# Optimization experiments

Measured on AMD Instinct MI355X. Metric: run time of the kernel, lower is better.

Reference implementation:

```python
import jax, jax.numpy as jnp
import numpy as np

B, N, M, C, H = 8, 2048, 1024, 512, 8
D = C // H  # per-head dim = 64


def setup_inputs() -> dict:
    key = jax.random.key(0)
    ks = jax.random.split(key, 4)
    x = jax.random.normal(ks[0], (B, N, C), dtype=jnp.float32)
    global_tokens = jax.random.normal(ks[1], (B, M, C), dtype=jnp.float32)
    Wq = jax.random.normal(ks[2], (C, C), dtype=jnp.float32) * 0.02
    bq = jnp.zeros((C,), dtype=jnp.float32)
    Wkv = jax.random.normal(ks[3], (C, 2 * C), dtype=jnp.float32) * 0.02
    bkv = jnp.zeros((2 * C,), dtype=jnp.float32)
    return {"x": x, "global_tokens": global_tokens, "Wq": Wq, "bq": bq,
            "Wkv": Wkv, "bkv": bkv}


def reference(x, global_tokens, Wq, bq, Wkv, bkv):
    # q from x, k/v from global_tokens (LinearProjection with query=True)
    q = (x @ Wq + bq).reshape(B, N, H, D).transpose(0, 2, 1, 3)        # [B,H,N,D]
    kv = (global_tokens @ Wkv + bkv).reshape(B, M, 2, H, D)
    k = kv[:, :, 0].transpose(0, 2, 1, 3)                              # [B,H,M,D]
    v = kv[:, :, 1].transpose(0, 2, 1, 3)                              # [B,H,M,D]
    # NOTE: original module applies no 1/sqrt(D) scaling in forward
    attn = jnp.einsum('bhnd,bhmd->bhnm', q, k)                         # [B,H,N,M]
    attn = jax.nn.softmax(attn, axis=-1)
    out = jnp.einsum('bhnm,bhmd->bhnd', attn, v)                       # [B,H,N,D]
    return out.transpose(0, 2, 1, 3).reshape(B, N, C)
```

## Files before the change

kernel.cpp:

```cpp
#include <hip/hip_runtime.h>
#include <hip/hip_bf16.h>


typedef __bf16 bf16_t;
typedef __bf16 bf16x8 __attribute__((ext_vector_type(8)));
typedef __bf16 bf16x4 __attribute__((ext_vector_type(4)));
typedef float floatx16 __attribute__((ext_vector_type(16)));
typedef unsigned int uintx4 __attribute__((ext_vector_type(4)));
typedef unsigned int uintx2 __attribute__((ext_vector_type(2)));

#define KDIM 512
#define QSCALE 1.44269504088896f

__device__ __forceinline__ unsigned pack2(float a, float b) {
  unsigned short ua = __builtin_bit_cast(unsigned short, (bf16_t)a);
  unsigned short ub = __builtin_bit_cast(unsigned short, (bf16_t)b);
  return (unsigned)ua | ((unsigned)ub << 16);
}

__device__ __forceinline__ float fexp2(float x) {
#if __has_builtin(__builtin_amdgcn_exp2f)
  return __builtin_amdgcn_exp2f(x);
#else
  return __exp2f(x);
#endif
}

__device__ __forceinline__ bf16x8 cvt8(const float4 a, const float4 b) {
  bf16x8 r;
  r[0] = (bf16_t)a.x; r[1] = (bf16_t)a.y; r[2] = (bf16_t)a.z; r[3] = (bf16_t)a.w;
  r[4] = (bf16_t)b.x; r[5] = (bf16_t)b.y; r[6] = (bf16_t)b.z; r[7] = (bf16_t)b.w;
  return r;
}

__device__ __forceinline__ void gl_lds16(const bf16_t* g, bf16_t* l) {
#if __has_builtin(__builtin_amdgcn_global_load_lds)
  __builtin_amdgcn_global_load_lds(
      (const __attribute__((address_space(1))) unsigned int*)(g),
      (__attribute__((address_space(3))) unsigned int*)(l), 16, 0, 0);
#else
  *(bf16x8*)l = *(const bf16x8*)g;
#endif
}

__global__ __launch_bounds__(256) void prep_kernel(
    const float* __restrict__ Wq, const float* __restrict__ Wkv,
    const float* __restrict__ x, const float* __restrict__ gt,
    bf16_t* __restrict__ Wqt, bf16_t* __restrict__ Wkvt,
    bf16_t* __restrict__ Aq, bf16_t* __restrict__ Akv) {
  __shared__ float tile[64][65];
  const int blk = blockIdx.x;
  const int t = threadIdx.x;
  if (blk < 192) {
    const float* in; bf16_t* out; int N, bx, by;
    if (blk < 64) { in = Wq; out = Wqt; N = 512; bx = blk & 7; by = blk >> 3; }
    else { int t2 = blk - 64; in = Wkv; out = Wkvt; N = 1024; bx = t2 & 15; by = t2 >> 4; }
    const int c0 = bx * 64, k0 = by * 64;
#pragma unroll
    for (int i = 0; i < 16; ++i) {
      int idx = t + i * 256;
      int kk = idx >> 6, cc = idx & 63;
      tile[kk][cc] = in[(size_t)(k0 + kk) * N + (c0 + cc)];
    }
    __syncthreads();
#pragma unroll
    for (int j = 0; j < 2; ++j) {
      int unit = t + j * 256;
      int cc = unit >> 3, ks = (unit & 7) * 8;
      int c = c0 + cc, k = k0 + ks;
      bf16x8 v;
#pragma unroll
      for (int i = 0; i < 8; ++i) v[i] = (bf16_t)tile[ks + i][cc];
      const int k5 = k & 31;
      const int chunk = ((c & 127) >> 5) * 2 + (k5 >> 4);
      *(bf16x8*)(&out[(size_t)((c >> 7) * 16 + (k >> 5)) * 4096 + chunk * 512 +
                      (c & 31) * 8 + ((k5 >> 3) & 1) * 256]) = v;
    }
  } else {
    int idx = blk - 192;
    const float* src; bf16_t* dst; int rt, kt2;
    if (idx < 2048) { src = x; dst = Aq; rt = idx >> 4; kt2 = idx & 15; }
    else { int i2 = idx - 2048; src = gt; dst = Akv; rt = i2 >> 4; kt2 = i2 & 15; }
    const int row = rt * 128 + (t >> 1);
    const int kb = kt2 * 32 + (t & 1) * 16;
    const float* p = src + (size_t)row * KDIM + kb;
    float4 f0 = *(const float4*)(p);
    float4 f1 = *(const float4*)(p + 4);
    float4 f2 = *(const float4*)(p + 8);
    float4 f3 = *(const float4*)(p + 12);
    bf16x8 o0 = cvt8(f0, f1), o1 = cvt8(f2, f3);
    const int chunk = ((row & 127) >> 5) * 2 + (t & 1);
    bf16_t* ob = dst + (size_t)(rt * 16 + kt2) * 4096 + chunk * 512 + (row & 31) * 8;
    *(bf16x8*)(ob) = o0;
    *(bf16x8*)(ob + 256) = o1;
  }
}

__global__ __launch_bounds__(256) void proj_gemm_kernel(
    const bf16_t* __restrict__ Aq, const bf16_t* __restrict__ Akv,
    const bf16_t* __restrict__ Wqt, const bf16_t* __restrict__ Wkvt,
    const float* __restrict__ bq, const float* __restrict__ bkv,
    bf16_t* __restrict__ Qf, bf16_t* __restrict__ Kf, bf16_t* __restrict__ Vf) {
  __shared__ bf16_t lds[2][8192];
  const int blk = blockIdx.x;
  int mode, bx, by;
  const bf16_t* Ab; const bf16_t* Wb; const float* bias;
  if (blk < 512) { mode = 0; bx = blk & 3; by = blk >> 2; Ab = Aq; Wb = Wqt; bias = bq; }
  else { int tt = blk - 512; mode = 1; bx = tt & 7; by = tt >> 3; Ab = Akv; Wb = Wkvt; bias = bkv; }

  const int tid = threadIdx.x;
  const int wave = tid >> 6, L = tid & 63;
  const int l5 = L & 31, hf = L >> 5;
  const int wr = wave >> 1, wc = wave & 1;
  const int rb = by * 128, cb = bx * 128;

  const bf16_t* Abase = Ab + (size_t)by * 16 * 4096 + L * 8;
  const bf16_t* Wbase = Wb + (size_t)bx * 16 * 4096 + L * 8;

  auto dma = [&](int buf, int kt) {
#pragma unroll
    for (int j = 0; j < 4; ++j) {
      const int s = wave * 4 + j;
      const bf16_t* g = (s < 8) ? (Abase + (size_t)kt * 4096 + s * 512)
                                : (Wbase + (size_t)kt * 4096 + (s - 8) * 512);
      gl_lds16(g, &lds[buf][(s < 8 ? s * 512 : 4096 + (s - 8) * 512) + L * 8]);
    }
  };

  dma(0, 0);
  __syncthreads();

  floatx16 acc[2][2] = {};
  for (int kt = 0; kt < 16; ++kt) {
    const int cur = kt & 1;
    if (kt < 15) dma(cur ^ 1, kt + 1);
    bf16x8 af[2][2], wf[2][2];
#pragma unroll
    for (int rs = 0; rs < 2; ++rs)
#pragma unroll
      for (int kh = 0; kh < 2; ++kh)
        af[rs][kh] = *(const bf16x8*)(&lds[cur][((wr * 2 + rs) * 2 + kh) * 512 + L * 8]);
#pragma unroll
    for (int cs = 0; cs < 2; ++cs)
#pragma unroll
      for (int kh = 0; kh < 2; ++kh)
        wf[cs][kh] = *(const bf16x8*)(&lds[cur][4096 + ((wc * 2 + cs) * 2 + kh) * 512 + L * 8]);
#pragma unroll
    for (int rs = 0; rs < 2; ++rs)
#pragma unroll
      for (int cs = 0; cs < 2; ++cs)
#pragma unroll
        for (int kh = 0; kh < 2; ++kh)
          acc[rs][cs] = __builtin_amdgcn_mfma_f32_32x32x16_bf16(
              af[rs][kh], wf[cs][kh], acc[rs][cs], 0, 0, 0);
    __syncthreads();
  }

#pragma unroll
  for (int rs = 0; rs < 2; ++rs)
#pragma unroll
    for (int cs = 0; cs < 2; ++cs) {
      const int col = cb + wc * 64 + cs * 32 + l5;
      const float bv = bias[col];
      const int grb = rb + wr * 64 + rs * 32;
      if (mode == 0) {
        const int hh = col >> 6, d = col & 63;
        const int dof = (d >> 3) * 256 + (d & 7);
#pragma unroll
        for (int r = 0; r < 16; ++r) {
          int gr = grb + (r & 3) + 8 * (r >> 2) + 4 * hf;
          int b = gr >> 11, n = gr & 2047;
          Qf[(size_t)(b * 8 + hh) * 131072 + (n >> 5) * 2048 + dof + (n & 31) * 8] =
              (bf16_t)((acc[rs][cs][r] + bv) * QSCALE);
        }
      } else if (col < 512) {
        const int hh = col >> 6, d = col & 63;
        const int dof = (d >> 3) * 256 + (d & 7);
#pragma unroll
        for (int r = 0; r < 16; ++r) {
          int gr = grb + (r & 3) + 8 * (r >> 2) + 4 * hf;
          int b = gr >> 10, m = gr & 1023;
          Kf[(size_t)(b * 8 + hh) * 65536 + (m >> 5) * 2048 + dof + (m & 31) * 8] =
              (bf16_t)(acc[rs][cs][r] + bv);
        }
      } else {
        const int cc = col - 512;
        const int hh = cc >> 6, d = cc & 63;
        const int dof = (d >> 5) * 1024 + (d & 31) * 8;
#pragma unroll
        for (int rq = 0; rq < 4; ++rq) {
          int gr = grb + 8 * rq + 4 * hf;
          int b = gr >> 10, m = gr & 1023;
          bf16x4 pk;
          pk[0] = (bf16_t)(acc[rs][cs][rq * 4 + 0] + bv);
          pk[1] = (bf16_t)(acc[rs][cs][rq * 4 + 1] + bv);
          pk[2] = (bf16_t)(acc[rs][cs][rq * 4 + 2] + bv);
          pk[3] = (bf16_t)(acc[rs][cs][rq * 4 + 3] + bv);
          *(bf16x4*)(&Vf[(size_t)(b * 8 + hh) * 65536 + (m >> 5) * 2048 + dof +
                         ((m >> 4) & 1) * 512 + ((m >> 3) & 1) * 256 + (m & 7)]) = pk;
        }
      }
    }
}

__global__ __launch_bounds__(256, 4) void flash_attn_kernel(
    const bf16_t* __restrict__ Qf, const bf16_t* __restrict__ Kf,
    const bf16_t* __restrict__ Vf, float* __restrict__ out) {
  __shared__ bf16_t kv[2][2][4096];
  const int tid = threadIdx.x;
  const int wave = tid >> 6, L = tid & 63;
  const int l5 = L & 31, hf = L >> 5;
  const int bh = blockIdx.y;
  const int b = bh >> 3, hh = bh & 7;
  const int nb = blockIdx.x * 128 + wave * 32;

  const bf16_t* Qp = Qf + (size_t)bh * 131072 + (nb >> 5) * 2048 + L * 8;
  const bf16_t* Kb = Kf + (size_t)bh * 65536 + L * 8;
  const bf16_t* Vb = Vf + (size_t)bh * 65536 + L * 8;

  bf16x8 qf[4];
#pragma unroll
  for (int kc = 0; kc < 4; ++kc) qf[kc] = *(const bf16x8*)(Qp + kc * 512);

  bf16x8 ones;
#pragma unroll
  for (int i = 0; i < 8; ++i) ones[i] = (bf16_t)1.0f;

  floatx16 o0 = {}, o1 = {}, lacc = {};

  auto dma = [&](int buf, int ep2) {
#pragma unroll
    for (int j = 0; j < 4; ++j) {
      const int s = wave * 4 + j;
      const int sub = s >> 3, q = s & 7;
      const bf16_t* g = (q < 4) ? (Kb + (size_t)(ep2 * 2 + sub) * 2048 + q * 512)
                                : (Vb + (size_t)(ep2 * 2 + sub) * 2048 + (q - 4) * 512);
      bf16_t* l = &kv[buf][sub][(q < 4 ? q * 512 : 2048 + (q - 4) * 512) + L * 8];
      gl_lds16(g, l);
    }
  };

  dma(0, 0);
  __syncthreads();

  for (int ep = 0; ep < 16; ++ep) {
    const int cur = ep & 1;
    if (ep < 15) dma(cur ^ 1, ep + 1);
#pragma unroll
    for (int sub = 0; sub < 2; ++sub) {
      const bf16_t* kb = &kv[cur][sub][L * 8];
      const bf16_t* vb = &kv[cur][sub][2048 + L * 8];
      bf16x8 kf4[4];
#pragma unroll
      for (int kc = 0; kc < 4; ++kc) kf4[kc] = *(const bf16x8*)(kb + kc * 512);
      floatx16 sa = {};
#pragma unroll
      for (int kc = 0; kc < 4; ++kc)
        sa = __builtin_amdgcn_mfma_f32_32x32x16_bf16(kf4[kc], qf[kc], sa, 0, 0, 0);
      bf16x8 vf4[4];
#pragma unroll
      for (int j = 0; j < 4; ++j) vf4[j] = *(const bf16x8*)(vb + j * 512);
      unsigned w[8];
#pragma unroll
      for (int i = 0; i < 8; ++i) {
        float pa = fexp2(sa[2 * i]), pb = fexp2(sa[2 * i + 1]);
        w[i] = pack2(pa, pb);
      }
      uintx4 fw0, fw1;
#if __has_builtin(__builtin_amdgcn_permlane32_swap)
      {
        uintx2 r0 = __builtin_amdgcn_permlane32_swap(w[0], w[2], false, false);
        uintx2 r1 = __builtin_amdgcn_permlane32_swap(w[1], w[3], false, false);
        uintx2 r2 = __builtin_amdgcn_permlane32_swap(w[4], w[6], false, false);
        uintx2 r3 = __builtin_amdgcn_permlane32_swap(w[5], w[7], false, false);
        fw0.x = r0[0]; fw0.z = r0[1];
        fw0.y = r1[0]; fw0.w = r1[1];
        fw1.x = r2[0]; fw1.z = r2[1];
        fw1.y = r3[0]; fw1.w = r3[1];
      }
#else
      {
        unsigned sw[8];
#pragma unroll
        for (int i = 0; i < 8; ++i) sw[i] = __shfl_xor(w[i], 32);
        fw0.x = hf ? sw[2] : w[0]; fw0.y = hf ? sw[3] : w[1];
        fw0.z = hf ? w[2] : sw[0]; fw0.w = hf ? w[3] : sw[1];
        fw1.x = hf ? sw[6] : w[4]; fw1.y = hf ? sw[7] : w[5];
        fw1.z = hf ? w[6] : sw[4]; fw1.w = hf ? w[7] : sw[5];
      }
#endif
      bf16x8 pf0 = __builtin_bit_cast(bf16x8, fw0);
      bf16x8 pf1 = __builtin_bit_cast(bf16x8, fw1);
      lacc = __builtin_amdgcn_mfma_f32_32x32x16_bf16(ones, pf0, lacc, 0, 0, 0);
      lacc = __builtin_amdgcn_mfma_f32_32x32x16_bf16(ones, pf1, lacc, 0, 0, 0);
      o0 = __builtin_amdgcn_mfma_f32_32x32x16_bf16(vf4[0], pf0, o0, 0, 0, 0);
      o0 = __builtin_amdgcn_mfma_f32_32x32x16_bf16(vf4[1], pf1, o0, 0, 0, 0);
      o1 = __builtin_amdgcn_mfma_f32_32x32x16_bf16(vf4[2], pf0, o1, 0, 0, 0);
      o1 = __builtin_amdgcn_mfma_f32_32x32x16_bf16(vf4[3], pf1, o1, 0, 0, 0);
    }
    __syncthreads();
  }

  const float inv = 1.0f / lacc[0];

  float* lob = (float*)(&kv[0][0][0]) + wave * (32 * 36);
  const size_t orow = (size_t)b * 2048 + nb;
#pragma unroll
  for (int pass = 0; pass < 2; ++pass) {
    const floatx16& oo = pass ? o1 : o0;
#pragma unroll
    for (int i = 0; i < 8; ++i) {
      const int d = 2 * (i & 1) + 8 * (i >> 1) + 4 * hf;
      float2 a;
      a.x = oo[2 * i] * inv; a.y = oo[2 * i + 1] * inv;
      *(float2*)(&lob[l5 * 36 + d]) = a;
    }
#pragma unroll
    for (int j = 0; j < 4; ++j) {
      int chunk = j * 64 + L;
      int n = chunk >> 3, c = chunk & 7;
      float4 v = *(const float4*)(&lob[n * 36 + c * 4]);
      *(float4*)(&out[(orow + n) * 512 + hh * 64 + pass * 32 + c * 4]) = v;
    }
  }
}

extern "C" void kernel_launch(void* const* d_in, const int* in_sizes, int n_in,
                              void* d_out, int out_size, void* d_ws, size_t ws_size,
                              hipStream_t stream) {
  (void)in_sizes; (void)n_in; (void)out_size; (void)ws_size;
  const float* x   = (const float*)d_in[0];
  const float* gt  = (const float*)d_in[1];
  const float* Wq  = (const float*)d_in[2];
  const float* bq  = (const float*)d_in[3];
  const float* Wkv = (const float*)d_in[4];
  const float* bkv = (const float*)d_in[5];
  float* out = (float*)d_out;

  bf16_t* Wqt  = (bf16_t*)d_ws;
  bf16_t* Wkvt = Wqt + (size_t)512 * 512;
  bf16_t* Qf   = Wkvt + (size_t)1024 * 512;
  bf16_t* Kf   = Qf + (size_t)64 * 2048 * 64;
  bf16_t* Vf   = Kf + (size_t)64 * 1024 * 64;
  bf16_t* Aq   = (bf16_t*)d_out;
  bf16_t* Akv  = Aq + (size_t)16384 * 512;

  prep_kernel<<<3264, 256, 0, stream>>>(Wq, Wkv, x, gt, Wqt, Wkvt, Aq, Akv);
  proj_gemm_kernel<<<1024, 256, 0, stream>>>(Aq, Akv, Wqt, Wkvt, bq, bkv, Qf, Kf, Vf);
  flash_attn_kernel<<<dim3(16, 64), 256, 0, stream>>>(Qf, Kf, Vf, out);
}
```

Measured before the change: 179.1 us.

## Deepen LDS prefetch pipelines with vmcnt-based waits and MFMA priority

The projection GEMM moves from double to triple buffering, prefetching two k-tiles ahead. The attention kernel moves from double-buffered pairs of KV subtiles to a four-slot ring of single subtiles, prefetching three ahead. Both kernels now wait on explicit s_waitcnt vmcnt counts plus a single barrier per step, where they previously used full __syncthreads. MFMA sections are wrapped in s_setprio to favour math issue. The aim is to hide global-to-LDS latency better, at the cost of more LDS in the GEMM and fragile hand-tuned wait counts.

```diff
diff --git a/kernel.cpp b/kernel.cpp
--- a/kernel.cpp
+++ b/kernel.cpp
@@ -11,6 +11,13 @@
 
 #define KDIM 512
 #define QSCALE 1.44269504088896f
+
+#define WAITVM(N) asm volatile("s_waitcnt vmcnt(" #N ")" ::: "memory")
+#define BAR()                                  \
+  do {                                         \
+    __builtin_amdgcn_s_barrier();              \
+    asm volatile("" ::: "memory");             \
+  } while (0)
 
 __device__ __forceinline__ unsigned pack2(float a, float b) {
   unsigned short ua = __builtin_bit_cast(unsigned short, (bf16_t)a);
@@ -101,7 +108,7 @@
     const bf16_t* __restrict__ Wqt, const bf16_t* __restrict__ Wkvt,
     const float* __restrict__ bq, const float* __restrict__ bkv,
     bf16_t* __restrict__ Qf, bf16_t* __restrict__ Kf, bf16_t* __restrict__ Vf) {
-  __shared__ bf16_t lds[2][8192];
+  __shared__ bf16_t lds[3][8192];
   const int blk = blockIdx.x;
   int mode, bx, by;
   const bf16_t* Ab; const bf16_t* Wb; const float* bias;
@@ -127,13 +134,9 @@
     }
   };
 
-  dma(0, 0);
-  __syncthreads();
-
   floatx16 acc[2][2] = {};
-  for (int kt = 0; kt < 16; ++kt) {
-    const int cur = kt & 1;
-    if (kt < 15) dma(cur ^ 1, kt + 1);
+
+  auto kstep = [&](int cur) {
     bf16x8 af[2][2], wf[2][2];
 #pragma unroll
     for (int rs = 0; rs < 2; ++rs)
@@ -145,6 +148,7 @@
 #pragma unroll
       for (int kh = 0; kh < 2; ++kh)
         wf[cs][kh] = *(const bf16x8*)(&lds[cur][4096 + ((wc * 2 + cs) * 2 + kh) * 512 + L * 8]);
+    __builtin_amdgcn_s_setprio(1);
 #pragma unroll
     for (int rs = 0; rs < 2; ++rs)
 #pragma unroll
@@ -153,8 +157,26 @@
         for (int kh = 0; kh < 2; ++kh)
           acc[rs][cs] = __builtin_amdgcn_mfma_f32_32x32x16_bf16(
               af[rs][kh], wf[cs][kh], acc[rs][cs], 0, 0, 0);
-    __syncthreads();
+    __builtin_amdgcn_s_setprio(0);
+  };
+
+  dma(0, 0);
+  dma(1, 1);
+
+  int cur = 0, pf = 2;
+  for (int kt = 0; kt < 15; ++kt) {
+    WAITVM(4);
+    BAR();
+    if (kt <= 13) {
+      dma(pf, kt + 2);
+      pf = (pf == 2) ? 0 : pf + 1;
+    }
+    kstep(cur);
+    cur = (cur == 2) ? 0 : cur + 1;
   }
+  WAITVM(0);
+  BAR();
+  kstep(cur);
 
 #pragma unroll
   for (int rs = 0; rs < 2; ++rs)
@@ -206,7 +228,7 @@
 __global__ __launch_bounds__(256, 4) void flash_attn_kernel(
     const bf16_t* __restrict__ Qf, const bf16_t* __restrict__ Kf,
     const bf16_t* __restrict__ Vf, float* __restrict__ out) {
-  __shared__ bf16_t kv[2][2][4096];
+  __shared__ bf16_t kv[4][4096];
   const int tid = threadIdx.x;
   const int wave = tid >> 6, L = tid & 63;
   const int l5 = L & 31, hf = L >> 5;
@@ -228,82 +250,94 @@
 
   floatx16 o0 = {}, o1 = {}, lacc = {};
 
-  auto dma = [&](int buf, int ep2) {
-#pragma unroll
-    for (int j = 0; j < 4; ++j) {
-      const int s = wave * 4 + j;
-      const int sub = s >> 3, q = s & 7;
-      const bf16_t* g = (q < 4) ? (Kb + (size_t)(ep2 * 2 + sub) * 2048 + q * 512)
-                                : (Vb + (size_t)(ep2 * 2 + sub) * 2048 + (q - 4) * 512);
-      bf16_t* l = &kv[buf][sub][(q < 4 ? q * 512 : 2048 + (q - 4) * 512) + L * 8];
-      gl_lds16(g, l);
+  auto dma = [&](int buf, int s) {
+#pragma unroll
+    for (int j = 0; j < 2; ++j) {
+      const int q = wave * 2 + j;
+      const bf16_t* g = (q < 4) ? (Kb + (size_t)s * 2048 + q * 512)
+                                : (Vb + (size_t)s * 2048 + (q - 4) * 512);
+      gl_lds16(g, &kv[buf][(q < 4 ? q * 512 : 2048 + (q - 4) * 512) + L * 8]);
     }
   };
 
+  auto subtile = [&](int s) {
+    const bf16_t* kb = &kv[s & 3][L * 8];
+    const bf16_t* vb = &kv[s & 3][2048 + L * 8];
+    bf16x8 kf4[4];
+#pragma unroll
+    for (int kc = 0; kc < 4; ++kc) kf4[kc] = *(const bf16x8*)(kb + kc * 512);
+    floatx16 sa = {};
+    __builtin_amdgcn_s_setprio(1);
+#pragma unroll
+    for (int kc = 0; kc < 4; ++kc)
+      sa = __builtin_amdgcn_mfma_f32_32x32x16_bf16(kf4[kc], qf[kc], sa, 0, 0, 0);
+    __builtin_amdgcn_s_setprio(0);
+    bf16x8 vf4[4];
+#pragma unroll
+    for (int j = 0; j < 4; ++j) vf4[j] = *(const bf16x8*)(vb + j * 512);
+    unsigned w[8];
+#pragma unroll
+    for (int i = 0; i < 8; ++i) {
+      float pa = fexp2(sa[2 * i]), pb = fexp2(sa[2 * i + 1]);
+      w[i] = pack2(pa, pb);
+    }
+    uintx4 fw0, fw1;
+#if __has_builtin(__builtin_amdgcn_permlane32_swap)
+    {
+      uintx2 r0 = __builtin_amdgcn_permlane32_swap(w[0], w[2], false, false);
+      uintx2 r1 = __builtin_amdgcn_permlane32_swap(w[1], w[3], false, false);
+      uintx2 r2 = __builtin_amdgcn_permlane32_swap(w[4], w[6], false, false);
+      uintx2 r3 = __builtin_amdgcn_permlane32_swap(w[5], w[7], false, false);
+      fw0.x = r0[0]; fw0.z = r0[1];
+      fw0.y = r1[0]; fw0.w = r1[1];
+      fw1.x = r2[0]; fw1.z = r2[1];
+      fw1.y = r3[0]; fw1.w = r3[1];
+    }
+#else
+    {
+      unsigned sw[8];
+#pragma unroll
+      for (int i = 0; i < 8; ++i) sw[i] = __shfl_xor(w[i], 32);
+      fw0.x = hf ? sw[2] : w[0]; fw0.y = hf ? sw[3] : w[1];
+      fw0.z = hf ? w[2] : sw[0]; fw0.w = hf ? w[3] : sw[1];
+      fw1.x = hf ? sw[6] : w[4]; fw1.y = hf ? sw[7] : w[5];
+      fw1.z = hf ? w[6] : sw[4]; fw1.w = hf ? w[7] : sw[5];
+    }
+#endif
+    bf16x8 pf0 = __builtin_bit_cast(bf16x8, fw0);
+    bf16x8 pf1 = __builtin_bit_cast(bf16x8, fw1);
+    __builtin_amdgcn_s_setprio(1);
+    lacc = __builtin_amdgcn_mfma_f32_32x32x16_bf16(ones, pf0, lacc, 0, 0, 0);
+    lacc = __builtin_amdgcn_mfma_f32_32x32x16_bf16(ones, pf1, lacc, 0, 0, 0);
+    o0 = __builtin_amdgcn_mfma_f32_32x32x16_bf16(vf4[0], pf0, o0, 0, 0, 0);
+    o0 = __builtin_amdgcn_mfma_f32_32x32x16_bf16(vf4[1], pf1, o0, 0, 0, 0);
+    o1 = __builtin_amdgcn_mfma_f32_32x32x16_bf16(vf4[2], pf0, o1, 0, 0, 0);
+    o1 = __builtin_amdgcn_mfma_f32_32x32x16_bf16(vf4[3], pf1, o1, 0, 0, 0);
+    __builtin_amdgcn_s_setprio(0);
+  };
+
   dma(0, 0);
+  dma(1, 1);
+  dma(2, 2);
+
+  for (int s = 0; s < 30; ++s) {
+    WAITVM(4);
+    BAR();
+    if (s <= 28) dma((s + 3) & 3, s + 3);
+    subtile(s);
+  }
+  WAITVM(2);
+  BAR();
+  subtile(30);
+  WAITVM(0);
+  BAR();
+  subtile(31);
+
   __syncthreads();
 
-  for (int ep = 0; ep < 16; ++ep) {
-    const int cur = ep & 1;
-    if (ep < 15) dma(cur ^ 1, ep + 1);
-#pragma unroll
-    for (int sub = 0; sub < 2; ++sub) {
-      const bf16_t* kb = &kv[cur][sub][L * 8];
-      const bf16_t* vb = &kv[cur][sub][2048 + L * 8];
-      bf16x8 kf4[4];
-#pragma unroll
-      for (int kc = 0; kc < 4; ++kc) kf4[kc] = *(const bf16x8*)(kb + kc * 512);
-      floatx16 sa = {};
-#pragma unroll
-      for (int kc = 0; kc < 4; ++kc)
-        sa = __builtin_amdgcn_mfma_f32_32x32x16_bf16(kf4[kc], qf[kc], sa, 0, 0, 0);
-      bf16x8 vf4[4];
-#pragma unroll
-      for (int j = 0; j < 4; ++j) vf4[j] = *(const bf16x8*)(vb + j * 512);
-      unsigned w[8];
-#pragma unroll
-      for (int i = 0; i < 8; ++i) {
-        float pa = fexp2(sa[2 * i]), pb = fexp2(sa[2 * i + 1]);
-        w[i] = pack2(pa, pb);
-      }
-      uintx4 fw0, fw1;
-#if __has_builtin(__builtin_amdgcn_permlane32_swap)
-      {
-        uintx2 r0 = __builtin_amdgcn_permlane32_swap(w[0], w[2], false, false);
-        uintx2 r1 = __builtin_amdgcn_permlane32_swap(w[1], w[3], false, false);
-        uintx2 r2 = __builtin_amdgcn_permlane32_swap(w[4], w[6], false, false);
-        uintx2 r3 = __builtin_amdgcn_permlane32_swap(w[5], w[7], false, false);
-        fw0.x = r0[0]; fw0.z = r0[1];
-        fw0.y = r1[0]; fw0.w = r1[1];
-        fw1.x = r2[0]; fw1.z = r2[1];
-        fw1.y = r3[0]; fw1.w = r3[1];
-      }
-#else
-      {
-        unsigned sw[8];
-#pragma unroll
-        for (int i = 0; i < 8; ++i) sw[i] = __shfl_xor(w[i], 32);
-        fw0.x = hf ? sw[2] : w[0]; fw0.y = hf ? sw[3] : w[1];
-        fw0.z = hf ? w[2] : sw[0]; fw0.w = hf ? w[3] : sw[1];
-        fw1.x = hf ? sw[6] : w[4]; fw1.y = hf ? sw[7] : w[5];
-        fw1.z = hf ? w[6] : sw[4]; fw1.w = hf ? w[7] : sw[5];
-      }
-#endif
-      bf16x8 pf0 = __builtin_bit_cast(bf16x8, fw0);
-      bf16x8 pf1 = __builtin_bit_cast(bf16x8, fw1);
-      lacc = __builtin_amdgcn_mfma_f32_32x32x16_bf16(ones, pf0, lacc, 0, 0, 0);
-      lacc = __builtin_amdgcn_mfma_f32_32x32x16_bf16(ones, pf1, lacc, 0, 0, 0);
-      o0 = __builtin_amdgcn_mfma_f32_32x32x16_bf16(vf4[0], pf0, o0, 0, 0, 0);
-      o0 = __builtin_amdgcn_mfma_f32_32x32x16_bf16(vf4[1], pf1, o0, 0, 0, 0);
-      o1 = __builtin_amdgcn_mfma_f32_32x32x16_bf16(vf4[2], pf0, o1, 0, 0, 0);
-      o1 = __builtin_amdgcn_mfma_f32_32x32x16_bf16(vf4[3], pf1, o1, 0, 0, 0);
-    }
-    __syncthreads();
-  }
-
   const float inv = 1.0f / lacc[0];
 
-  float* lob = (float*)(&kv[0][0][0]) + wave * (32 * 36);
+  float* lob = (float*)(&kv[0][0]) + wave * (32 * 36);
   const size_t orow = (size_t)b * 2048 + nb;
 #pragma unroll
   for (int pass = 0; pass < 2; ++pass) {
```

Measured after the change: 180.7 us. Within noise of the previous version (+0.9%).
